# Performance work log

Hardware: AMD Instinct MI355X
Metric: run time of the kernel (lower is better)

Reference implementation:

```python
import jax, jax.numpy as jnp
import numpy as np

HIDDEN = 4096
NUM_HEADS = 32
HEAD_DIM = 128
NUM_KV_HEADS = 8
KV_GROUPS = NUM_HEADS // NUM_KV_HEADS
ROPE_THETA = 10000.0
SEQ = 2048
BATCH = 1
NEG_INF = -1e9


def fake_quant_int8(x):
    """Per-tensor symmetric int8 fake quantization (absmax scale)."""
    scale = jnp.maximum(jnp.max(jnp.abs(x)) / 127.0, 1e-8)
    q = jnp.clip(jnp.round(x / scale), -127.0, 127.0) * scale
    # straight-through estimator (no-op in fwd-only, keeps code shared)
    return x + jax.lax.stop_gradient(q - x)


def rotate_half(x):
    x1, x2 = jnp.split(x, 2, axis=-1)
    return jnp.concatenate([-x2, x1], axis=-1)


def rope_cos_sin(position_ids):
    inv_freq = 1.0 / (ROPE_THETA ** (jnp.arange(0, HEAD_DIM, 2, dtype=jnp.float32) / HEAD_DIM))
    freqs = position_ids.astype(jnp.float32)[..., None] * inv_freq  # [B,S,HD/2]
    emb = jnp.concatenate([freqs, freqs], axis=-1)                  # [B,S,HD]
    return jnp.cos(emb), jnp.sin(emb)


def setup_inputs() -> dict:
    key = jax.random.key(0)
    k1, k2, k3, k4, k5 = jax.random.split(key, 5)
    hidden_states = jax.random.normal(k1, (BATCH, SEQ, HIDDEN), dtype=jnp.float32)
    causal = jnp.tril(jnp.ones((SEQ, SEQ), dtype=bool))
    attention_mask = jnp.where(causal, 0.0, NEG_INF).astype(jnp.float32)[None, None]  # [1,1,S,S]
    position_ids = jnp.arange(SEQ, dtype=jnp.int64 if jax.config.jax_enable_x64 else jnp.int32)[None, :]
    s = 0.02
    wq = jax.random.normal(k2, (NUM_HEADS * HEAD_DIM, HIDDEN), dtype=jnp.float32) * s
    wk = jax.random.normal(k3, (NUM_KV_HEADS * HEAD_DIM, HIDDEN), dtype=jnp.float32) * s
    wv = jax.random.normal(k4, (NUM_KV_HEADS * HEAD_DIM, HIDDEN), dtype=jnp.float32) * s
    wo = jax.random.normal(k5, (HIDDEN, NUM_HEADS * HEAD_DIM), dtype=jnp.float32) * s
    return {"hidden_states": hidden_states, "attention_mask": attention_mask,
            "position_ids": position_ids, "wq": wq, "wk": wk, "wv": wv, "wo": wo}


def reference(hidden_states, attention_mask, position_ids, wq, wk, wv, wo):
    B, S, _ = hidden_states.shape

    def qlinear(x, w):  # quantized linear: fake-quant act and weight, y = x @ w.T
        return fake_quant_int8(x) @ fake_quant_int8(w).T

    q = qlinear(hidden_states, wq).reshape(B, S, NUM_HEADS, HEAD_DIM).transpose(0, 2, 1, 3)
    k = qlinear(hidden_states, wk).reshape(B, S, NUM_KV_HEADS, HEAD_DIM).transpose(0, 2, 1, 3)
    v = qlinear(hidden_states, wv).reshape(B, S, NUM_KV_HEADS, HEAD_DIM).transpose(0, 2, 1, 3)

    cos, sin = rope_cos_sin(position_ids)      # [B,S,HD]
    cos, sin = cos[:, None], sin[:, None]      # [B,1,S,HD]
    q = q * cos + rotate_half(q) * sin
    k = k * cos + rotate_half(k) * sin

    # repeat_kv: GQA -> full heads
    k = jnp.repeat(k, KV_GROUPS, axis=1)
    v = jnp.repeat(v, KV_GROUPS, axis=1)

    # quantized QK^T
    scores = jnp.einsum('bhqd,bhkd->bhqk', fake_quant_int8(q), fake_quant_int8(k))
    scores = scores * (1.0 / np.sqrt(HEAD_DIM).astype(np.float32))
    scores = scores + attention_mask[:, :, :, :S]
    probs = jax.nn.softmax(scores.astype(jnp.float32), axis=-1).astype(q.dtype)
    # attention_dropout = 0.0 -> identity

    # quantized AV
    attn_out = jnp.einsum('bhqk,bhkd->bhqd', fake_quant_int8(probs), fake_quant_int8(v))
    attn_out = attn_out.transpose(0, 2, 1, 3).reshape(B, S, NUM_HEADS * HEAD_DIM)
    return qlinear(attn_out, wo)
```

## Files before the change

### kernel.cpp

```cpp
#include <hip/hip_runtime.h>
#include <hip/hip_fp16.h>
#include <stdint.h>

#define SEQ   2048
#define HID   4096
#define NH    32
#define NKV   8
#define KVDIM 1024
#define KVCAT 2048

typedef int v4i __attribute__((ext_vector_type(4)));

#define VMCNT0 asm volatile("s_waitcnt vmcnt(0)" ::: "memory")

__device__ __forceinline__ void gload16(const void* g, void* l) {
    __builtin_amdgcn_global_load_lds(
        (const __attribute__((address_space(1))) void*)(uintptr_t)g,
        (__attribute__((address_space(3))) void*)(uintptr_t)l, 16, 0, 0);
}

__device__ __forceinline__ float slot_scale(const unsigned* slots, int slot) {
    return fmaxf(__uint_as_float(slots[slot << 5]) / 127.0f, 1e-8f);
}

__device__ __forceinline__ int q8v(float x, float s) {
    int v = (int)rintf(x / s);
    return v < -127 ? -127 : (v > 127 ? 127 : v);
}

__device__ __forceinline__ unsigned pk4(float a, float b, float c, float d, float s) {
    return (unsigned)(uint8_t)(int8_t)q8v(a, s)
         | ((unsigned)(uint8_t)(int8_t)q8v(b, s) << 8)
         | ((unsigned)(uint8_t)(int8_t)q8v(c, s) << 16)
         | ((unsigned)(uint8_t)(int8_t)q8v(d, s) << 24);
}

__device__ __forceinline__ float fexp2(float x) {
    float r; asm("v_exp_f32 %0, %1" : "=v"(r) : "v"(x)); return r;
}

__device__ __forceinline__ float fmax4a(float4 x) {
    return fmaxf(fmaxf(fabsf(x.x), fabsf(x.y)), fmaxf(fabsf(x.z), fabsf(x.w)));
}

__device__ __forceinline__ void block_amax_part(float m, float* dst) {
    __shared__ float sm[4];
    int lane = threadIdx.x & 63, w = threadIdx.x >> 6;
    for (int off = 32; off; off >>= 1) m = fmaxf(m, __shfl_xor(m, off, 64));
    if (lane == 0) sm[w] = m;
    __syncthreads();
    if (threadIdx.x == 0)
        *dst = fmaxf(fmaxf(sm[0], sm[1]), fmaxf(sm[2], sm[3]));
    __syncthreads();
}

#define NV0 ((long)SEQ * HID / 4)
#define NV1 ((long)HID * HID / 4)
#define NV2 ((long)KVDIM * HID / 4)
__global__ void k_absmax5(const float* __restrict__ a0, const float* __restrict__ a1,
                          const float* __restrict__ a2, const float* __restrict__ a3,
                          const float* __restrict__ a4, float* __restrict__ part) {
    int b = blockIdx.x;
    const float* p; long n; int lb, nb;
    if (b < 342)       { p = a0; n = NV0; lb = b;        nb = 342; }
    else if (b < 1025) { p = a1; n = NV1; lb = b - 342;  nb = 683; }
    else if (b < 1196) { p = a2; n = NV2; lb = b - 1025; nb = 171; }
    else if (b < 1367) { p = a3; n = NV2; lb = b - 1196; nb = 171; }
    else               { p = a4; n = NV1; lb = b - 1367; nb = 681; }
    long str = (long)nb * 256;
    float mm[8] = {0.f, 0.f, 0.f, 0.f, 0.f, 0.f, 0.f, 0.f};
    long v = (long)lb * 256 + threadIdx.x;
    for (; v + 7 * str < n; v += 8 * str) {
        float4 t[8];
        #pragma unroll
        for (int j = 0; j < 8; j++) t[j] = *(const float4*)(p + (v + j * str) * 4);
        #pragma unroll
        for (int j = 0; j < 8; j++) mm[j] = fmaxf(mm[j], fmax4a(t[j]));
    }
    for (; v < n; v += str) mm[0] = fmaxf(mm[0], fmax4a(*(const float4*)(p + v * 4)));
    float m = fmaxf(fmaxf(fmaxf(mm[0], mm[1]), fmaxf(mm[2], mm[3])),
                    fmaxf(fmaxf(mm[4], mm[5]), fmaxf(mm[6], mm[7])));
    block_amax_part(m, part + blockIdx.x);
}

__global__ void k_reduceA(const float* __restrict__ part, unsigned* slots) {
    __shared__ float sm[4];
    const int lo[5] = {0, 342, 1025, 1196, 1367};
    const int hi[5] = {342, 1025, 1196, 1367, 2048};
    int t = threadIdx.x, lane = t & 63, w = t >> 6;
    for (int s = 0; s < 5; s++) {
        float m = 0.f;
        for (int i = lo[s] + t; i < hi[s]; i += 256) m = fmaxf(m, part[i]);
        for (int off = 32; off; off >>= 1) m = fmaxf(m, __shfl_xor(m, off, 64));
        if (lane == 0) sm[w] = m;
        __syncthreads();
        if (t == 0)
            slots[s << 5] = __float_as_uint(fmaxf(fmaxf(sm[0], sm[1]), fmaxf(sm[2], sm[3])));
        __syncthreads();
    }
}

__global__ void k_reduceB(const float* __restrict__ p1, const float* __restrict__ p2,
                          const float* __restrict__ p3, unsigned* slots) {
    __shared__ float sm[4];
    int t = threadIdx.x, lane = t & 63, w = t >> 6;
    const float* ps[3] = {p1, p2, p3};
    const int cnt[3] = {512, 128, 128};
    const int sl[3] = {5, 6, 7};
    for (int s = 0; s < 3; s++) {
        float m = 0.f;
        for (int i = t; i < cnt[s]; i += 256) m = fmaxf(m, ps[s][i]);
        for (int off = 32; off; off >>= 1) m = fmaxf(m, __shfl_xor(m, off, 64));
        if (lane == 0) sm[w] = m;
        __syncthreads();
        if (t == 0)
            slots[sl[s] << 5] = __float_as_uint(fmaxf(fmaxf(sm[0], sm[1]), fmaxf(sm[2], sm[3])));
        __syncthreads();
    }
}

#define NU0 ((long)SEQ * HID / 16)
#define NU1 ((long)HID * HID / 16)
#define NU2 ((long)KVDIM * HID / 16)
__global__ void k_quant5(const float* __restrict__ a0, const float* __restrict__ a1,
                         const float* __restrict__ a2, const float* __restrict__ a3,
                         const float* __restrict__ a4,
                         int8_t* __restrict__ d0, int8_t* __restrict__ d1,
                         int8_t* __restrict__ d2, int8_t* __restrict__ d3,
                         int8_t* __restrict__ d4,
                         const unsigned* __restrict__ slots) {
    int b = blockIdx.x;
    const float* p; int8_t* d; long n; int slot, lb, nb;
    if (b < 512)       { p = a0; d = d0; n = NU0; slot = 0; lb = b;        nb = 512; }
    else if (b < 1536) { p = a1; d = d1; n = NU1; slot = 1; lb = b - 512;  nb = 1024; }
    else if (b < 1792) { p = a2; d = d2; n = NU2; slot = 2; lb = b - 1536; nb = 256; }
    else if (b < 2048) { p = a3; d = d3; n = NU2; slot = 3; lb = b - 1792; nb = 256; }
    else               { p = a4; d = d4; n = NU1; slot = 4; lb = b - 2048; nb = 512; }
    float s = slot_scale(slots, slot);
    long str = (long)nb * 256;
    for (long u = (long)lb * 256 + threadIdx.x; u < n; u += str) {
        const float4* src = (const float4*)(p + u * 16);
        float4 t0 = src[0], t1 = src[1], t2 = src[2], t3 = src[3];
        int4 o;
        o.x = (int)pk4(t0.x, t0.y, t0.z, t0.w, s);
        o.y = (int)pk4(t1.x, t1.y, t1.z, t1.w, s);
        o.z = (int)pk4(t2.x, t2.y, t2.z, t2.w, s);
        o.w = (int)pk4(t3.x, t3.y, t3.z, t3.w, s);
        *(int4*)(d + u * 16) = o;
    }
}

__device__ __forceinline__ unsigned pk4h(unsigned h2a, unsigned h2b, float s) {
    __half2 a = *(__half2*)&h2a, b = *(__half2*)&h2b;
    return pk4(__low2float(a), __high2float(a), __low2float(b), __high2float(b), s);
}
__global__ void k_quanth(const __half* __restrict__ x, int8_t* __restrict__ q, long nu,
                         int rshift, long cmask, long ld,
                         const unsigned* __restrict__ slots, int slot) {
    float s = slot_scale(slots, slot);
    long gs = (long)gridDim.x * blockDim.x;
    for (long u = blockIdx.x * (long)blockDim.x + threadIdx.x; u < nu; u += gs) {
        long row = u >> rshift;
        long cu = u & cmask;
        const int4* src = (const int4*)(x + row * ld + cu * 16);
        int4 a = src[0], b = src[1];
        int4 o;
        o.x = (int)pk4h((unsigned)a.x, (unsigned)a.y, s);
        o.y = (int)pk4h((unsigned)a.z, (unsigned)a.w, s);
        o.z = (int)pk4h((unsigned)b.x, (unsigned)b.y, s);
        o.w = (int)pk4h((unsigned)b.z, (unsigned)b.w, s);
        *(int4*)(q + u * 16) = o;
    }
}

__global__ void k_ropetab(const int* __restrict__ pos, float* __restrict__ ct,
                          float* __restrict__ st) {
    int tid = blockIdx.x * blockDim.x + threadIdx.x;
    if (tid >= SEQ * 64) return;
    int i = tid & 63, s = tid >> 6;
    double inv = 1.0 / pow(10000.0, (double)((float)(2 * i) * (1.0f / 128.0f)));
    float invf = (float)inv;
    float angf = (float)pos[s] * invf;
    double a = (double)angf;
    ct[tid] = (float)cos(a);
    st[tid] = (float)sin(a);
}

__global__ void k_transq(const __half* __restrict__ src, long lds_, int8_t* __restrict__ dst,
                         long ldd, const unsigned* __restrict__ slots, int slot) {
    __shared__ float t[32][33];
    float s = slot_scale(slots, slot);
    int bx = blockIdx.x, by = blockIdx.y;
    int tid = threadIdx.x;
    int c = tid & 31, r0 = tid >> 5;
    #pragma unroll
    for (int j = 0; j < 4; j++) {
        int r = r0 + j * 8;
        t[r][c] = __half2float(src[(long)(by * 32 + r) * lds_ + bx * 32 + c]);
    }
    __syncthreads();
    int d = tid >> 3, k4 = (tid & 7) * 4;
    unsigned pa = 0;
    #pragma unroll
    for (int j = 0; j < 4; j++) {
        int iv = q8v(t[k4 + j][d], s);
        pa |= ((unsigned)(uint8_t)(int8_t)iv) << (8 * j);
    }
    *(unsigned*)(dst + (long)(bx * 32 + d) * ldd + by * 32 + k4) = pa;
}

__global__ __launch_bounds__(256) void k_gemm_i8(
    const int8_t* __restrict__ A, const int8_t* __restrict__ B, void* __restrict__ Cv,
    int N, int K, unsigned* slots,
    int slotA, int slotB, int slotB2, int nsplit,
    float* pQ, float* pK, float* pV, int ropemode,
    const float* __restrict__ ct, const float* __restrict__ st) {
    __shared__ int8_t POOL[65536];
    int8_t (*As)[16384] = (int8_t(*)[16384])POOL;
    int8_t (*Bs)[16384] = (int8_t(*)[16384])(POOL + 32768);
    float* Cf = (float*)Cv;
    __half* Ch = (__half*)Cv;
    const v4i vzero = {0, 0, 0, 0};
    int tid = threadIdx.x, lane = tid & 63, wid = tid >> 6;
    int nbx = N >> 7;
    int nwg = gridDim.x, wg = blockIdx.x;
    int cpx = nwg >> 3;
    int swz = (wg & 7) * cpx + (wg >> 3);
    int bm = swz / nbx, bn = swz % nbx;
    long rowA0 = (long)bm * 128, colB0 = (long)bn * 128;
    int wrow = (wid >> 1) * 64, wcol = (wid & 1) * 64;
    int lr = lane >> 3;
    int swc = ((lane & 7) ^ lr) * 16;
    const int8_t* ga = A + (rowA0 + wid * 8 + lr) * (long)K + swc;
    const int8_t* gb = B + (colB0 + wid * 8 + lr) * (long)K + swc;
    v4i acc[4][4];
    #pragma unroll
    for (int m = 0; m < 4; m++)
        #pragma unroll
        for (int n = 0; n < 4; n++) acc[m][n] = vzero;

    auto STAGE = [&](int buf, int kt) {
        #pragma unroll
        for (int i = 0; i < 4; i++) {
            gload16(ga + kt + (long)(i * 32) * K, &As[buf][(wid * 8 + i * 32) * 128]);
            gload16(gb + kt + (long)(i * 32) * K, &Bs[buf][(wid * 8 + i * 32) * 128]);
        }
    };
    auto COMPUTE = [&](int buf) {
        #pragma unroll
        for (int ks = 0; ks < 2; ks++) {
            v4i af[4], bf[4];
            #pragma unroll
            for (int m = 0; m < 4; m++) {
                int row = wrow + m * 16 + (lane & 15);
                af[m] = *(const v4i*)(&As[buf][row * 128 + (((ks * 4 + (lane >> 4)) ^ (row & 7)) * 16)]);
            }
            #pragma unroll
            for (int n = 0; n < 4; n++) {
                int row = wcol + n * 16 + (lane & 15);
                bf[n] = *(const v4i*)(&Bs[buf][row * 128 + (((ks * 4 + (lane >> 4)) ^ (row & 7)) * 16)]);
            }
            #pragma unroll
            for (int m = 0; m < 4; m++)
                #pragma unroll
                for (int n = 0; n < 4; n++)
                    acc[m][n] = __builtin_amdgcn_mfma_i32_16x16x64_i8(af[m], bf[n], acc[m][n], 0, 0, 0);
        }
    };

    STAGE(0, 0);
    VMCNT0;
    __syncthreads();
    int nt = K >> 7, cur = 0;
    for (int t = 0; t < nt - 1; t++) {
        STAGE(cur ^ 1, (t + 1) << 7);
        COMPUTE(cur);
        VMCNT0;
        __syncthreads();
        cur ^= 1;
    }
    COMPUTE(cur);

    float sA = slot_scale(slots, slotA);
    float sB1 = slot_scale(slots, slotB);
    float sB2 = slot_scale(slots, slotB2);
    int qc = lane & 15, rgrp = (lane >> 4) << 2;
    if (ropemode == 1 || (ropemode == 2 && bn < 8)) {
        __syncthreads();
        float* EX = (float*)POOL;
        #pragma unroll
        for (int m = 0; m < 4; m++)
            #pragma unroll
            for (int n = 0; n < 4; n++) {
                int coll = wcol + n * 16 + qc;
                #pragma unroll
                for (int r = 0; r < 4; r++) {
                    int rowl = wrow + m * 16 + rgrp + r;
                    EX[rowl * 128 + (coll ^ ((rowl & 1) << 4))] = sA * sB1 * (float)acc[m][n][r];
                }
            }
        __syncthreads();
        float am = 0.f;
        #pragma unroll
        for (int m = 0; m < 4; m++)
            #pragma unroll
            for (int n = 0; n < 4; n++) {
                int coll = wcol + n * 16 + qc;
                #pragma unroll
                for (int r = 0; r < 4; r++) {
                    int rowl = wrow + m * 16 + rgrp + r;
                    long srow = rowA0 + rowl;
                    float self = EX[rowl * 128 + (coll ^ ((rowl & 1) << 4))];
                    float pv = EX[rowl * 128 + ((coll ^ 64) ^ ((rowl & 1) << 4))];
                    float c = ct[srow * 64 + (coll & 63)];
                    float sn = st[srow * 64 + (coll & 63)];
                    float o = (coll < 64) ? self * c - pv * sn : self * c + pv * sn;
                    am = fmaxf(am, fabsf(o));
                    Ch[srow * N + colB0 + coll] = __float2half(o);
                }
            }
        block_amax_part(am, (ropemode == 1) ? pQ + blockIdx.x : pK + bm * 8 + (bn & 7));
    } else if (ropemode == 2) {
        float am = 0.f;
        #pragma unroll
        for (int m = 0; m < 4; m++) {
            long row0 = rowA0 + wrow + m * 16 + rgrp;
            #pragma unroll
            for (int n = 0; n < 4; n++) {
                int col = (int)colB0 + wcol + n * 16 + qc;
                float sc = sA * ((col < nsplit) ? sB1 : sB2);
                __half* cp = Ch + row0 * N + col;
                #pragma unroll
                for (int r = 0; r < 4; r++) {
                    float val = sc * (float)acc[m][n][r];
                    cp[(long)r * N] = __float2half(val);
                    am = fmaxf(am, fabsf(val));
                }
            }
        }
        block_amax_part(am, pV + bm * 8 + (bn & 7));
    } else {
        #pragma unroll
        for (int m = 0; m < 4; m++) {
            long row0 = rowA0 + wrow + m * 16 + rgrp;
            #pragma unroll
            for (int n = 0; n < 4; n++) {
                int col = (int)colB0 + wcol + n * 16 + qc;
                float sc = sA * ((col < nsplit) ? sB1 : sB2);
                float* cp = Cf + row0 * N + col;
                #pragma unroll
                for (int r = 0; r < 4; r++) cp[(long)r * N] = sc * (float)acc[m][n][r];
            }
        }
    }
}

__global__ __launch_bounds__(256) void k_attn(
    const int8_t* __restrict__ Qq, const int8_t* __restrict__ Kq, const int8_t* __restrict__ Vtq,
    __half* __restrict__ AO, unsigned* slots) {
    __shared__ int8_t Qs[64 * 128];
    __shared__ int8_t Ks[2][64 * 128];
    __shared__ int8_t Vs[2][128 * 64];
    __shared__ int smx[4];
    __shared__ int tmx[4][32][16];
    const v4i vzero = {0, 0, 0, 0};
    const int NEGS = -(1 << 29);
    const float MAGIC = 12582912.0f;
    int tid = threadIdx.x, lane = tid & 63, w = tid >> 6;
    int qlan = lane & 15, g = lane >> 4;
    int idx = blockIdx.x;
    int qb = 31 - (idx >> 5), h = idx & 31, kvh = h >> 2;
    float sq = slot_scale(slots, 5), sk = slot_scale(slots, 6);
    float spv = slot_scale(slots, 7) * (1.0f / 127.0f);
    float c2 = sq * sk * 0.08838834764831845f * 1.4426950408889634f;
    int lr8 = lane >> 3;
    int swc = ((lane & 7) ^ lr8) * 16;
    int lr4 = lane >> 2;
    int vswc = ((lane & 3) ^ (lr4 & 3)) * 16;
    const int8_t* kbase = Kq + ((long)(w * 8 + lr8)) * KVDIM + kvh * 128 + swc;
    const int8_t* vbase = Vtq + ((long)kvh * 128 + w * 16 + lr4) * SEQ + vswc;
    auto STAGE_K = [&](int buf, int kt) {
        #pragma unroll
        for (int i = 0; i < 2; i++)
            gload16(kbase + ((long)kt * 64 + i * 32) * KVDIM, &Ks[buf][(w * 8 + i * 32) * 128]);
    };
    auto STAGE_V = [&](int buf, int kt) {
        #pragma unroll
        for (int i = 0; i < 2; i++)
            gload16(vbase + (long)(i * 64) * SEQ + kt * 64, &Vs[buf][(w * 16 + i * 64) * 64]);
    };
    {
        const int8_t* qbase = Qq + ((long)qb * 64 + w * 8 + lr8) * HID + h * 128 + swc;
        #pragma unroll
        for (int i = 0; i < 2; i++)
            gload16(qbase + (long)(i * 32) * HID, &Qs[(w * 8 + i * 32) * 128]);
    }
    STAGE_K(0, 0);
    VMCNT0;
    __syncthreads();
    v4i aq[2];
    #pragma unroll
    for (int ks = 0; ks < 2; ks++) {
        int row = w * 16 + qlan;
        aq[ks] = *(const v4i*)(&Qs[row * 128 + (((ks * 4 + g) ^ (row & 7)) * 16)]);
    }
    int mi = -(1 << 30);
    float l = 0.f;
    int buf = 0;
    for (int kt = 0; kt <= qb; kt++) {
        if (kt < qb) STAGE_K(buf ^ 1, kt + 1);
        v4i sf[4] = {vzero, vzero, vzero, vzero};
        __builtin_amdgcn_s_setprio(1);
        #pragma unroll
        for (int ks = 0; ks < 2; ks++)
            #pragma unroll
            for (int f = 0; f < 4; f++) {
                int row = f * 16 + qlan;
                v4i bk = *(const v4i*)(&Ks[buf][row * 128 + (((ks * 4 + g) ^ (row & 7)) * 16)]);
                sf[f] = __builtin_amdgcn_mfma_i32_16x16x64_i8(bk, aq[ks], sf[f], 0, 0, 0);
            }
        __builtin_amdgcn_s_setprio(0);
        int sv[16];
        if (kt == qb) {
            int qthr = w * 16 + qlan;
            #pragma unroll
            for (int f = 0; f < 4; f++)
                #pragma unroll
                for (int r = 0; r < 4; r++) {
                    int kl = f * 16 + g * 4 + r;
                    sv[f * 4 + r] = (kl > qthr) ? NEGS : sf[f][r];
                }
        } else {
            #pragma unroll
            for (int f = 0; f < 4; f++)
                #pragma unroll
                for (int r = 0; r < 4; r++) sv[f * 4 + r] = sf[f][r];
        }
        int tm = sv[0];
        #pragma unroll
        for (int e = 1; e < 16; e++) tm = tm > sv[e] ? tm : sv[e];
        tm = max(tm, __shfl_xor(tm, 16, 64));
        tm = max(tm, __shfl_xor(tm, 32, 64));
        tmx[w][kt][qlan] = tm;
        int mn = tm > mi ? tm : mi;
        float nb = -c2 * (float)mn;
        float esc = fexp2(fmaf((float)mi, c2, nb));
        float es = 0.f;
        #pragma unroll
        for (int e = 0; e < 16; e++) es += fexp2(fmaf((float)sv[e], c2, nb));
        es += __shfl_xor(es, 16, 64);
        es += __shfl_xor(es, 32, 64);
        l = l * esc + es;
        mi = mn;
        VMCNT0;
        __syncthreads();
        buf ^= 1;
    }
    float Bq = fmaf(c2, (float)mi, __log2f(l) - 6.9886846867721655f);
    unsigned* Ps32 = (unsigned*)Qs;
    int pwr = w * 320;
    v4i of[8];
    #pragma unroll
    for (int nf = 0; nf < 8; nf++) of[nf] = vzero;
    STAGE_K(0, 0);
    STAGE_V(0, 0);
    VMCNT0;
    __syncthreads();
    buf = 0;
    for (int kt = 0; kt <= qb; kt++) {
        if (kt < qb) { STAGE_K(buf ^ 1, kt + 1); STAGE_V(buf ^ 1, kt + 1); }
        int tmv = tmx[w][kt][qlan];
        int act = (fmaf(c2, (float)tmv, -Bq) > -1.0f);
        if (__any(act)) {
            v4i sf[4] = {vzero, vzero, vzero, vzero};
            __builtin_amdgcn_s_setprio(1);
            #pragma unroll
            for (int ks = 0; ks < 2; ks++)
                #pragma unroll
                for (int f = 0; f < 4; f++) {
                    int row = f * 16 + qlan;
                    v4i bk = *(const v4i*)(&Ks[buf][row * 128 + (((ks * 4 + g) ^ (row & 7)) * 16)]);
                    sf[f] = __builtin_amdgcn_mfma_i32_16x16x64_i8(bk, aq[ks], sf[f], 0, 0, 0);
                }
            __builtin_amdgcn_s_setprio(0);
            if (kt == qb) {
                int qthr = w * 16 + qlan;
                #pragma unroll
                for (int f = 0; f < 4; f++) {
                    unsigned pk = 0;
                    #pragma unroll
                    for (int r = 0; r < 4; r++) {
                        int kl = f * 16 + g * 4 + r;
                        int s = (kl > qthr) ? NEGS : sf[f][r];
                        float t = fexp2(fmaf((float)s, c2, -Bq));
                        unsigned u = __float_as_uint(t + MAGIC) & 127u;
                        pk |= u << (8 * r);
                    }
                    Ps32[pwr + (4 * f + g) * 20 + qlan] = pk;
                }
            } else {
                #pragma unroll
                for (int f = 0; f < 4; f++) {
                    unsigned pk = 0;
                    #pragma unroll
                    for (int r = 0; r < 4; r++) {
                        float t = fexp2(fmaf((float)sf[f][r], c2, -Bq));
                        unsigned u = __float_as_uint(t + MAGIC) & 127u;
                        pk |= u << (8 * r);
                    }
                    Ps32[pwr + (4 * f + g) * 20 + qlan] = pk;
                }
            }
            int rb = pwr + 80 * g + qlan;
            v4i ap;
            ap[0] = (int)Ps32[rb];
            ap[1] = (int)Ps32[rb + 20];
            ap[2] = (int)Ps32[rb + 40];
            ap[3] = (int)Ps32[rb + 60];
            __builtin_amdgcn_s_setprio(1);
            #pragma unroll
            for (int nf = 0; nf < 8; nf++) {
                int row = nf * 16 + qlan;
                v4i bv = *(const v4i*)(&Vs[buf][row * 64 + ((g ^ (row & 3)) * 16)]);
                of[nf] = __builtin_amdgcn_mfma_i32_16x16x64_i8(ap, bv, of[nf], 0, 0, 0);
            }
            __builtin_amdgcn_s_setprio(0);
        }
        VMCNT0;
        __syncthreads();
        buf ^= 1;
    }
    int mymax = 0;
    #pragma unroll
    for (int nf = 0; nf < 8; nf++)
        #pragma unroll
        for (int r = 0; r < 4; r++) {
            int val = of[nf][r];
            int av = val < 0 ? -val : val;
            mymax = av > mymax ? av : mymax;
            int qg = qb * 64 + w * 16 + 4 * g + r;
            AO[(long)qg * HID + h * 128 + nf * 16 + qlan] = __float2half(spv * (float)val);
        }
    #pragma unroll
    for (int off = 1; off < 64; off <<= 1) {
        int o2 = __shfl_xor(mymax, off, 64);
        mymax = o2 > mymax ? o2 : mymax;
    }
    if (lane == 0) smx[w] = mymax;
    __syncthreads();
    if (tid == 0) {
        int mm = max(max(smx[0], smx[1]), max(smx[2], smx[3]));
        atomicMax(slots + (8 << 5), (unsigned)mm);
    }
}

__global__ void k_quant_ao(const __half* __restrict__ a, int8_t* __restrict__ q,
                           unsigned* slots) {
    float sv = slot_scale(slots, 7);
    float spv = (1.0f / 127.0f) * sv;
    float amax = spv * (float)(int)slots[8 << 5];
    float s = fmaxf(amax / 127.0f, 1e-8f);
    long nu = (long)SEQ * HID / 16;
    long gs = (long)gridDim.x * blockDim.x;
    for (long u = blockIdx.x * (long)blockDim.x + threadIdx.x; u < nu; u += gs) {
        const int4* src = (const int4*)(a + u * 16);
        int4 x = src[0], y = src[1];
        int4 o;
        o.x = (int)pk4h((unsigned)x.x, (unsigned)x.y, s);
        o.y = (int)pk4h((unsigned)x.z, (unsigned)x.w, s);
        o.z = (int)pk4h((unsigned)y.x, (unsigned)y.y, s);
        o.w = (int)pk4h((unsigned)y.z, (unsigned)y.w, s);
        *(int4*)(q + u * 16) = o;
    }
    if (blockIdx.x == 0 && threadIdx.x == 0) slots[9 << 5] = __float_as_uint(amax);
}

extern "C" void kernel_launch(void* const* d_in, const int* in_sizes, int n_in,
                              void* d_out, int out_size, void* d_ws, size_t ws_size,
                              hipStream_t stream) {
    (void)in_sizes; (void)n_in; (void)out_size;
    const float* hid = (const float*)d_in[0];
    const int* pos = (const int*)d_in[2];
    const float* wqp = (const float*)d_in[3];
    const float* wkp = (const float*)d_in[4];
    const float* wvp = (const float*)d_in[5];
    const float* wop = (const float*)d_in[6];
    float* out = (float*)d_out;
    char* ws = (char*)d_ws;

    size_t o = 0;
    auto alloc = [&](size_t sz) { size_t r = o; o += (sz + 255) & ~(size_t)255; return r; };
    unsigned* slots = (unsigned*)(ws + alloc(2048));
    float* P0 = (float*)(ws + alloc(2048 * 4));
    float* P1 = (float*)(ws + alloc(512 * 4));
    float* P2 = (float*)(ws + alloc(128 * 4));
    float* P3 = (float*)(ws + alloc(128 * 4));
    int8_t* Xq   = (int8_t*)(ws + alloc((size_t)SEQ * HID));
    int8_t* Wqq  = (int8_t*)(ws + alloc((size_t)HID * HID));
    int8_t* Woq  = (int8_t*)(ws + alloc((size_t)HID * HID));
    int8_t* Wkvq = (int8_t*)(ws + alloc((size_t)KVCAT * HID));
    __half* Qf   = (__half*)(ws + alloc((size_t)SEQ * HID * 2));
    __half* KVf  = (__half*)(ws + alloc((size_t)SEQ * KVCAT * 2));
    int8_t* Qq   = (int8_t*)(ws + alloc((size_t)SEQ * HID));
    int8_t* Kq   = (int8_t*)(ws + alloc((size_t)SEQ * KVDIM));
    int8_t* Vtq  = (int8_t*)(ws + alloc((size_t)KVDIM * SEQ));
    float*  ctab = (float*)(ws + alloc((size_t)SEQ * 64 * 4));
    float*  stab = (float*)(ws + alloc((size_t)SEQ * 64 * 4));
    if (ws_size < o) return;
    __half* AOh = Qf;
    int8_t* AOq = Xq;

    hipMemsetAsync(slots, 0, 2048, stream);
    k_ropetab<<<SEQ * 64 / 256, 256, 0, stream>>>(pos, ctab, stab);
    k_absmax5<<<2048, 256, 0, stream>>>(hid, wqp, wkp, wvp, wop, P0);
    k_reduceA<<<1, 256, 0, stream>>>(P0, slots);
    k_quant5<<<2560, 256, 0, stream>>>(hid, wqp, wkp, wvp, wop,
                                       Xq, Wqq, Wkvq, Wkvq + (size_t)KVDIM * HID, Woq, slots);
    k_gemm_i8<<<512, 256, 0, stream>>>(Xq, Wqq, Qf, HID, HID, slots,
                                       0, 1, 1, 1 << 30, P1, nullptr, nullptr, 1, ctab, stab);
    k_gemm_i8<<<256, 256, 0, stream>>>(Xq, Wkvq, KVf, KVCAT, HID, slots,
                                       0, 2, 3, KVDIM, nullptr, P2, P3, 2, ctab, stab);
    k_reduceB<<<1, 256, 0, stream>>>(P1, P2, P3, slots);
    const long CALL = 0x3FFFFFFFL;
    k_quanth<<<1024, 256, 0, stream>>>(Qf, Qq, (long)SEQ * HID / 16, 40, CALL, 0, slots, 5);
    k_quanth<<<512, 256, 0, stream>>>(KVf, Kq, (long)SEQ * KVDIM / 16, 6, 63, KVCAT, slots, 6);
    k_transq<<<dim3(32, 64), 256, 0, stream>>>(KVf + KVDIM, KVCAT, Vtq, SEQ, slots, 7);
    k_attn<<<1024, 256, 0, stream>>>(Qq, Kq, Vtq, AOh, slots);
    k_quant_ao<<<1024, 256, 0, stream>>>(AOh, AOq, slots);
    k_gemm_i8<<<512, 256, 0, stream>>>(AOq, Woq, out, HID, HID, slots,
                                       9, 4, 4, 1 << 30, nullptr, nullptr, nullptr, 0,
                                       nullptr, nullptr);
}
```

Baseline: 291.8 us.

## Halve GEMM K-tile and shrink LDS with new swizzle; drop attention tile skipping

```diff
diff --git a/kernel.cpp b/kernel.cpp
--- a/kernel.cpp
+++ b/kernel.cpp
@@ -17,6 +17,15 @@
     __builtin_amdgcn_global_load_lds(
         (const __attribute__((address_space(1))) void*)(uintptr_t)g,
         (__attribute__((address_space(3))) void*)(uintptr_t)l, 16, 0, 0);
+}
+
+__device__ __forceinline__ int prsw(int row, int c) {
+    return (row >> 1) * 8 + (row & 1) * 4 + (c ^ ((row >> 1) & 3));
+}
+__device__ __forceinline__ void prsw_inv(int d, int& row, int& c) {
+    int rp = d >> 3, rem = d & 7;
+    row = 2 * rp + (rem >> 2);
+    c = (rem & 3) ^ (rp & 3);
 }
 
 __device__ __forceinline__ float slot_scale(const unsigned* slots, int slot) {
@@ -215,13 +224,14 @@
     int slotA, int slotB, int slotB2, int nsplit,
     float* pQ, float* pK, float* pV, int ropemode,
     const float* __restrict__ ct, const float* __restrict__ st) {
-    __shared__ int8_t POOL[65536];
-    int8_t (*As)[16384] = (int8_t(*)[16384])POOL;
-    int8_t (*Bs)[16384] = (int8_t(*)[16384])(POOL + 32768);
+    __shared__ int8_t POOL[32768];
+    int8_t (*As)[8192] = (int8_t(*)[8192])POOL;
+    int8_t (*Bs)[8192] = (int8_t(*)[8192])(POOL + 16384);
     float* Cf = (float*)Cv;
     __half* Ch = (__half*)Cv;
     const v4i vzero = {0, 0, 0, 0};
     int tid = threadIdx.x, lane = tid & 63, wid = tid >> 6;
+    int qlan = lane & 15, g = lane >> 4;
     int nbx = N >> 7;
     int nwg = gridDim.x, wg = blockIdx.x;
     int cpx = nwg >> 3;
@@ -229,51 +239,52 @@
     int bm = swz / nbx, bn = swz % nbx;
     long rowA0 = (long)bm * 128, colB0 = (long)bn * 128;
     int wrow = (wid >> 1) * 64, wcol = (wid & 1) * 64;
-    int lr = lane >> 3;
-    int swc = ((lane & 7) ^ lr) * 16;
-    const int8_t* ga = A + (rowA0 + wid * 8 + lr) * (long)K + swc;
-    const int8_t* gb = B + (colB0 + wid * 8 + lr) * (long)K + swc;
+    int r0_, c0_, r1_, c1_;
+    prsw_inv(tid, r0_, c0_);
+    prsw_inv(tid + 256, r1_, c1_);
+    const int8_t* sA0 = A + (rowA0 + r0_) * (long)K + c0_ * 16;
+    const int8_t* sA1 = A + (rowA0 + r1_) * (long)K + c1_ * 16;
+    const int8_t* sB0 = B + (colB0 + r0_) * (long)K + c0_ * 16;
+    const int8_t* sB1 = B + (colB0 + r1_) * (long)K + c1_ * 16;
     v4i acc[4][4];
     #pragma unroll
     for (int m = 0; m < 4; m++)
         #pragma unroll
         for (int n = 0; n < 4; n++) acc[m][n] = vzero;
+    int aoff[4], boff[4];
+    #pragma unroll
+    for (int m = 0; m < 4; m++) {
+        int row = wrow + m * 16 + qlan;
+        aoff[m] = prsw(row, g) * 16;
+        int rowb = wcol + m * 16 + qlan;
+        boff[m] = prsw(rowb, g) * 16;
+    }
 
     auto STAGE = [&](int buf, int kt) {
-        #pragma unroll
-        for (int i = 0; i < 4; i++) {
-            gload16(ga + kt + (long)(i * 32) * K, &As[buf][(wid * 8 + i * 32) * 128]);
-            gload16(gb + kt + (long)(i * 32) * K, &Bs[buf][(wid * 8 + i * 32) * 128]);
-        }
+        gload16(sA0 + kt, &As[buf][wid * 1024]);
+        gload16(sA1 + kt, &As[buf][wid * 1024 + 4096]);
+        gload16(sB0 + kt, &Bs[buf][wid * 1024]);
+        gload16(sB1 + kt, &Bs[buf][wid * 1024 + 4096]);
     };
     auto COMPUTE = [&](int buf) {
-        #pragma unroll
-        for (int ks = 0; ks < 2; ks++) {
-            v4i af[4], bf[4];
-            #pragma unroll
-            for (int m = 0; m < 4; m++) {
-                int row = wrow + m * 16 + (lane & 15);
-                af[m] = *(const v4i*)(&As[buf][row * 128 + (((ks * 4 + (lane >> 4)) ^ (row & 7)) * 16)]);
-            }
-            #pragma unroll
-            for (int n = 0; n < 4; n++) {
-                int row = wcol + n * 16 + (lane & 15);
-                bf[n] = *(const v4i*)(&Bs[buf][row * 128 + (((ks * 4 + (lane >> 4)) ^ (row & 7)) * 16)]);
-            }
-            #pragma unroll
-            for (int m = 0; m < 4; m++)
-                #pragma unroll
-                for (int n = 0; n < 4; n++)
-                    acc[m][n] = __builtin_amdgcn_mfma_i32_16x16x64_i8(af[m], bf[n], acc[m][n], 0, 0, 0);
-        }
+        v4i af[4], bf[4];
+        #pragma unroll
+        for (int m = 0; m < 4; m++) af[m] = *(const v4i*)(&As[buf][aoff[m]]);
+        #pragma unroll
+        for (int n = 0; n < 4; n++) bf[n] = *(const v4i*)(&Bs[buf][boff[n]]);
+        #pragma unroll
+        for (int m = 0; m < 4; m++)
+            #pragma unroll
+            for (int n = 0; n < 4; n++)
+                acc[m][n] = __builtin_amdgcn_mfma_i32_16x16x64_i8(af[m], bf[n], acc[m][n], 0, 0, 0);
     };
 
     STAGE(0, 0);
     VMCNT0;
     __syncthreads();
-    int nt = K >> 7, cur = 0;
+    int nt = K >> 6, cur = 0;
     for (int t = 0; t < nt - 1; t++) {
-        STAGE(cur ^ 1, (t + 1) << 7);
+        STAGE(cur ^ 1, (t + 1) << 6);
         COMPUTE(cur);
         VMCNT0;
         __syncthreads();
@@ -282,12 +293,12 @@
     COMPUTE(cur);
 
     float sA = slot_scale(slots, slotA);
-    float sB1 = slot_scale(slots, slotB);
-    float sB2 = slot_scale(slots, slotB2);
-    int qc = lane & 15, rgrp = (lane >> 4) << 2;
+    float sB1s = slot_scale(slots, slotB);
+    float sB2s = slot_scale(slots, slotB2);
+    int qc = qlan, rgrp = g << 2;
     if (ropemode == 1 || (ropemode == 2 && bn < 8)) {
         __syncthreads();
-        float* EX = (float*)POOL;
+        __half* EXh = (__half*)POOL;
         #pragma unroll
         for (int m = 0; m < 4; m++)
             #pragma unroll
@@ -296,7 +307,8 @@
                 #pragma unroll
                 for (int r = 0; r < 4; r++) {
                     int rowl = wrow + m * 16 + rgrp + r;
-                    EX[rowl * 128 + (coll ^ ((rowl & 1) << 4))] = sA * sB1 * (float)acc[m][n][r];
+                    EXh[rowl * 128 + (coll ^ ((rowl & 1) << 4))] =
+                        __float2half(sA * sB1s * (float)acc[m][n][r]);
                 }
             }
         __syncthreads();
@@ -310,8 +322,8 @@
                 for (int r = 0; r < 4; r++) {
                     int rowl = wrow + m * 16 + rgrp + r;
                     long srow = rowA0 + rowl;
-                    float self = EX[rowl * 128 + (coll ^ ((rowl & 1) << 4))];
-                    float pv = EX[rowl * 128 + ((coll ^ 64) ^ ((rowl & 1) << 4))];
+                    float self = __half2float(EXh[rowl * 128 + (coll ^ ((rowl & 1) << 4))]);
+                    float pv = __half2float(EXh[rowl * 128 + ((coll ^ 64) ^ ((rowl & 1) << 4))]);
                     float c = ct[srow * 64 + (coll & 63)];
                     float sn = st[srow * 64 + (coll & 63)];
                     float o = (coll < 64) ? self * c - pv * sn : self * c + pv * sn;
@@ -328,7 +340,7 @@
             #pragma unroll
             for (int n = 0; n < 4; n++) {
                 int col = (int)colB0 + wcol + n * 16 + qc;
-                float sc = sA * ((col < nsplit) ? sB1 : sB2);
+                float sc = sA * ((col < nsplit) ? sB1s : sB2s);
                 __half* cp = Ch + row0 * N + col;
                 #pragma unroll
                 for (int r = 0; r < 4; r++) {
@@ -346,7 +358,7 @@
             #pragma unroll
             for (int n = 0; n < 4; n++) {
                 int col = (int)colB0 + wcol + n * 16 + qc;
-                float sc = sA * ((col < nsplit) ? sB1 : sB2);
+                float sc = sA * ((col < nsplit) ? sB1s : sB2s);
                 float* cp = Cf + row0 * N + col;
                 #pragma unroll
                 for (int r = 0; r < 4; r++) cp[(long)r * N] = sc * (float)acc[m][n][r];
@@ -358,11 +370,10 @@
 __global__ __launch_bounds__(256) void k_attn(
     const int8_t* __restrict__ Qq, const int8_t* __restrict__ Kq, const int8_t* __restrict__ Vtq,
     __half* __restrict__ AO, unsigned* slots) {
-    __shared__ int8_t Qs[64 * 128];
     __shared__ int8_t Ks[2][64 * 128];
     __shared__ int8_t Vs[2][128 * 64];
+    __shared__ unsigned Ps[4 * 320];
     __shared__ int smx[4];
-    __shared__ int tmx[4][32][16];
     const v4i vzero = {0, 0, 0, 0};
     const int NEGS = -(1 << 29);
     const float MAGIC = 12582912.0f;
@@ -375,25 +386,27 @@
     float c2 = sq * sk * 0.08838834764831845f * 1.4426950408889634f;
     int lr8 = lane >> 3;
     int swc = ((lane & 7) ^ lr8) * 16;
-    int lr4 = lane >> 2;
-    int vswc = ((lane & 3) ^ (lr4 & 3)) * 16;
     const int8_t* kbase = Kq + ((long)(w * 8 + lr8)) * KVDIM + kvh * 128 + swc;
-    const int8_t* vbase = Vtq + ((long)kvh * 128 + w * 16 + lr4) * SEQ + vswc;
+    int vr0_, vc0_, vr1_, vc1_;
+    prsw_inv(tid, vr0_, vc0_);
+    prsw_inv(tid + 256, vr1_, vc1_);
+    const int8_t* sV0 = Vtq + ((long)kvh * 128 + vr0_) * SEQ + vc0_ * 16;
+    const int8_t* sV1 = Vtq + ((long)kvh * 128 + vr1_) * SEQ + vc1_ * 16;
     auto STAGE_K = [&](int buf, int kt) {
         #pragma unroll
         for (int i = 0; i < 2; i++)
             gload16(kbase + ((long)kt * 64 + i * 32) * KVDIM, &Ks[buf][(w * 8 + i * 32) * 128]);
     };
     auto STAGE_V = [&](int buf, int kt) {
-        #pragma unroll
-        for (int i = 0; i < 2; i++)
-            gload16(vbase + (long)(i * 64) * SEQ + kt * 64, &Vs[buf][(w * 16 + i * 64) * 64]);
+        gload16(sV0 + kt * 64, &Vs[buf][w * 1024]);
+        gload16(sV1 + kt * 64, &Vs[buf][w * 1024 + 4096]);
     };
     {
+        int8_t* Qstage = &Vs[0][0];
         const int8_t* qbase = Qq + ((long)qb * 64 + w * 8 + lr8) * HID + h * 128 + swc;
         #pragma unroll
         for (int i = 0; i < 2; i++)
-            gload16(qbase + (long)(i * 32) * HID, &Qs[(w * 8 + i * 32) * 128]);
+            gload16(qbase + (long)(i * 32) * HID, &Qstage[(w * 8 + i * 32) * 128]);
     }
     STAGE_K(0, 0);
     VMCNT0;
@@ -402,8 +415,9 @@
     #pragma unroll
     for (int ks = 0; ks < 2; ks++) {
         int row = w * 16 + qlan;
-        aq[ks] = *(const v4i*)(&Qs[row * 128 + (((ks * 4 + g) ^ (row & 7)) * 16)]);
-    }
+        aq[ks] = *(const v4i*)(&Vs[0][row * 128 + (((ks * 4 + g) ^ (row & 7)) * 16)]);
+    }
+    __syncthreads();
     int mi = -(1 << 30);
     float l = 0.f;
     int buf = 0;
@@ -441,7 +455,6 @@
         for (int e = 1; e < 16; e++) tm = tm > sv[e] ? tm : sv[e];
         tm = max(tm, __shfl_xor(tm, 16, 64));
         tm = max(tm, __shfl_xor(tm, 32, 64));
-        tmx[w][kt][qlan] = tm;
         int mn = tm > mi ? tm : mi;
         float nb = -c2 * (float)mn;
         float esc = fexp2(fmaf((float)mi, c2, nb));
@@ -457,7 +470,6 @@
         buf ^= 1;
     }
     float Bq = fmaf(c2, (float)mi, __log2f(l) - 6.9886846867721655f);
-    unsigned* Ps32 = (unsigned*)Qs;
     int pwr = w * 320;
     v4i of[8];
     #pragma unroll
@@ -469,63 +481,59 @@
     buf = 0;
     for (int kt = 0; kt <= qb; kt++) {
         if (kt < qb) { STAGE_K(buf ^ 1, kt + 1); STAGE_V(buf ^ 1, kt + 1); }
-        int tmv = tmx[w][kt][qlan];
-        int act = (fmaf(c2, (float)tmv, -Bq) > -1.0f);
-        if (__any(act)) {
-            v4i sf[4] = {vzero, vzero, vzero, vzero};
-            __builtin_amdgcn_s_setprio(1);
-            #pragma unroll
-            for (int ks = 0; ks < 2; ks++)
-                #pragma unroll
-                for (int f = 0; f < 4; f++) {
-                    int row = f * 16 + qlan;
-                    v4i bk = *(const v4i*)(&Ks[buf][row * 128 + (((ks * 4 + g) ^ (row & 7)) * 16)]);
-                    sf[f] = __builtin_amdgcn_mfma_i32_16x16x64_i8(bk, aq[ks], sf[f], 0, 0, 0);
+        v4i sf[4] = {vzero, vzero, vzero, vzero};
+        __builtin_amdgcn_s_setprio(1);
+        #pragma unroll
+        for (int ks = 0; ks < 2; ks++)
+            #pragma unroll
+            for (int f = 0; f < 4; f++) {
+                int row = f * 16 + qlan;
+                v4i bk = *(const v4i*)(&Ks[buf][row * 128 + (((ks * 4 + g) ^ (row & 7)) * 16)]);
+                sf[f] = __builtin_amdgcn_mfma_i32_16x16x64_i8(bk, aq[ks], sf[f], 0, 0, 0);
+            }
+        __builtin_amdgcn_s_setprio(0);
+        if (kt == qb) {
+            int qthr = w * 16 + qlan;
+            #pragma unroll
+            for (int f = 0; f < 4; f++) {
+                unsigned pk = 0;
+                #pragma unroll
+                for (int r = 0; r < 4; r++) {
+                    int kl = f * 16 + g * 4 + r;
+                    int s = (kl > qthr) ? NEGS : sf[f][r];
+                    float t = fexp2(fmaf((float)s, c2, -Bq));
+                    unsigned u = __float_as_uint(t + MAGIC) & 127u;
+                    pk |= u << (8 * r);
                 }
-            __builtin_amdgcn_s_setprio(0);
-            if (kt == qb) {
-                int qthr = w * 16 + qlan;
-                #pragma unroll
-                for (int f = 0; f < 4; f++) {
-                    unsigned pk = 0;
-                    #pragma unroll
-                    for (int r = 0; r < 4; r++) {
-                        int kl = f * 16 + g * 4 + r;
-                        int s = (kl > qthr) ? NEGS : sf[f][r];
-                        float t = fexp2(fmaf((float)s, c2, -Bq));
-                        unsigned u = __float_as_uint(t + MAGIC) & 127u;
-                        pk |= u << (8 * r);
-                    }
-                    Ps32[pwr + (4 * f + g) * 20 + qlan] = pk;
+                Ps[pwr + (4 * f + g) * 20 + qlan] = pk;
+            }
+        } else {
+            #pragma unroll
+            for (int f = 0; f < 4; f++) {
+                unsigned pk = 0;
+                #pragma unroll
+                for (int r = 0; r < 4; r++) {
+                    float t = fexp2(fmaf((float)sf[f][r], c2, -Bq));
+                    unsigned u = __float_as_uint(t + MAGIC) & 127u;
+                    pk |= u << (8 * r);
                 }
-            } else {
-                #pragma unroll
-                for (int f = 0; f < 4; f++) {
-                    unsigned pk = 0;
-                    #pragma unroll
-                    for (int r = 0; r < 4; r++) {
-                        float t = fexp2(fmaf((float)sf[f][r], c2, -Bq));
-                        unsigned u = __float_as_uint(t + MAGIC) & 127u;
-                        pk |= u << (8 * r);
-                    }
-                    Ps32[pwr + (4 * f + g) * 20 + qlan] = pk;
-                }
-            }
-            int rb = pwr + 80 * g + qlan;
-            v4i ap;
-            ap[0] = (int)Ps32[rb];
-            ap[1] = (int)Ps32[rb + 20];
-            ap[2] = (int)Ps32[rb + 40];
-            ap[3] = (int)Ps32[rb + 60];
-            __builtin_amdgcn_s_setprio(1);
-            #pragma unroll
-            for (int nf = 0; nf < 8; nf++) {
-                int row = nf * 16 + qlan;
-                v4i bv = *(const v4i*)(&Vs[buf][row * 64 + ((g ^ (row & 3)) * 16)]);
-                of[nf] = __builtin_amdgcn_mfma_i32_16x16x64_i8(ap, bv, of[nf], 0, 0, 0);
-            }
-            __builtin_amdgcn_s_setprio(0);
+                Ps[pwr + (4 * f + g) * 20 + qlan] = pk;
+            }
         }
+        int rb = pwr + 80 * g + qlan;
+        v4i ap;
+        ap[0] = (int)Ps[rb];
+        ap[1] = (int)Ps[rb + 20];
+        ap[2] = (int)Ps[rb + 40];
+        ap[3] = (int)Ps[rb + 60];
+        __builtin_amdgcn_s_setprio(1);
+        #pragma unroll
+        for (int nf = 0; nf < 8; nf++) {
+            int row = nf * 16 + qlan;
+            v4i bv = *(const v4i*)(&Vs[buf][prsw(row, g) * 16]);
+            of[nf] = __builtin_amdgcn_mfma_i32_16x16x64_i8(ap, bv, of[nf], 0, 0, 0);
+        }
+        __builtin_amdgcn_s_setprio(0);
         VMCNT0;
         __syncthreads();
         buf ^= 1;
@@ -610,7 +618,7 @@
     __half* AOh = Qf;
     int8_t* AOq = Xq;
 
-    hipMemsetAsync(slots, 0, 2048, stream);
+    (void)hipMemsetAsync(slots, 0, 2048, stream);
     k_ropetab<<<SEQ * 64 / 256, 256, 0, stream>>>(pos, ctab, stab);
     k_absmax5<<<2048, 256, 0, stream>>>(hid, wqp, wkp, wvp, wop, P0);
     k_reduceA<<<1, 256, 0, stream>>>(P0, slots);
```

Result: slower. 309.9 us (+6.2%).
